# Kernel tuning notes

Hardware: AMD Instinct MI355X
Metric: run time of the kernel (lower is better)

The kernel has to match this reference:

```python
import jax, jax.numpy as jnp
import numpy as np

T, D, I, E, K = 2048, 768, 2048, 8, 2


def setup_inputs() -> dict:
    key = jax.random.key(0)
    ks = jax.random.split(key, 9)
    x = jax.random.normal(ks[0], (T, D), jnp.float32)
    router_weight = jax.random.normal(ks[1], (E, D), jnp.float32) * 0.02
    shared_w_gate = jax.random.normal(ks[2], (I, D), jnp.float32) * 0.02
    shared_w_up = jax.random.normal(ks[3], (I, D), jnp.float32) * 0.02
    shared_w_down = jax.random.normal(ks[4], (D, I), jnp.float32) * 0.02
    # ternary quantized expert weights in {-1, 0, 1}
    expert_q_gate = jax.random.randint(ks[5], (E, I, D), 0, 3, jnp.int32) - 1
    expert_q_up = jax.random.randint(ks[6], (E, I, D), 0, 3, jnp.int32) - 1
    expert_q_down = jax.random.randint(ks[7], (E, D, I), 0, 3, jnp.int32) - 1
    # per-expert, per-matrix dequant scales (gate, up, down)
    expert_scales = jax.random.uniform(ks[8], (E, 3), jnp.float32) * 0.05 + 0.01
    return {
        "x": x,
        "router_weight": router_weight,
        "shared_w_gate": shared_w_gate,
        "shared_w_up": shared_w_up,
        "shared_w_down": shared_w_down,
        "expert_q_gate": expert_q_gate,
        "expert_q_up": expert_q_up,
        "expert_q_down": expert_q_down,
        "expert_scales": expert_scales,
        "top_k": K,
    }


def _swiglu(x, wg, wu, wd):
    # down( silu(gate(x)) * up(x) )
    return (jax.nn.silu(x @ wg.T) * (x @ wu.T)) @ wd.T


def reference(x, router_weight, shared_w_gate, shared_w_up, shared_w_down,
              expert_q_gate, expert_q_up, expert_q_down, expert_scales, top_k):
    # --- router: softmax -> top-k -> renormalize ---
    probs = jax.nn.softmax(x @ router_weight.T, axis=-1)            # [T, E]
    vals, idx = jax.lax.top_k(probs, top_k)                          # [T, K]
    vals = vals / jnp.sum(vals, axis=-1, keepdims=True)
    n_experts = router_weight.shape[0]
    # combine weights as dense [T, E] gate (one-hot scatter of top-k probs)
    gate = jnp.sum(jax.nn.one_hot(idx, n_experts, dtype=x.dtype) * vals[..., None], axis=1)

    # --- dequantize paged ternary experts: w = ternary * scale ---
    wg = expert_q_gate.astype(x.dtype) * expert_scales[:, 0, None, None]  # [E, I, D]
    wu = expert_q_up.astype(x.dtype) * expert_scales[:, 1, None, None]    # [E, I, D]
    wd = expert_q_down.astype(x.dtype) * expert_scales[:, 2, None, None]  # [E, D, I]

    # --- expert SwiGLU, computed per expert and combined with the gate ---
    h = jax.nn.silu(jnp.einsum('td,eid->tei', x, wg)) * jnp.einsum('td,eid->tei', x, wu)
    expert_out = jnp.einsum('tei,edi->ted', h, wd)                   # [T, E, D]
    moe_out = jnp.einsum('te,ted->td', gate, expert_out)             # [T, D]

    # --- always-on shared expert ---
    shared_out = _swiglu(x, shared_w_gate, shared_w_up, shared_w_down)
    return shared_out + moe_out
```

## Files before the change

### kernel.cpp

```cpp
#include <hip/hip_runtime.h>
#include <hip/hip_bf16.h>

#define TDIM 2048
#define DDIM 768
#define IDIM 2048
#define NEXP 8

typedef __bf16 v8bf __attribute__((ext_vector_type(8)));
typedef float v4f __attribute__((ext_vector_type(4)));
typedef int   v4i __attribute__((ext_vector_type(4)));
typedef float v4ff __attribute__((ext_vector_type(4)));

#define MFMA_B16(A,B,C) __builtin_amdgcn_mfma_f32_16x16x32_bf16(A,B,C,0,0,0)

typedef __attribute__((address_space(1))) const unsigned int* gas_t;
typedef __attribute__((address_space(3))) unsigned int* las_t;

__device__ __forceinline__ void gload16(const void* g, void* l) {
  __builtin_amdgcn_global_load_lds((gas_t)g, (las_t)l, 16, 0, 0);
}

__global__ __launch_bounds__(256)
void pack_all_kernel(const int* __restrict__ qg, const int* __restrict__ qu,
                     const int* __restrict__ qd,
                     const float* __restrict__ sg, const float* __restrict__ su,
                     const float* __restrict__ sd, const float* __restrict__ x,
                     const float* __restrict__ rw,
                     __hip_bfloat16* __restrict__ wgT, __hip_bfloat16* __restrict__ wuT,
                     __hip_bfloat16* __restrict__ wdT, __hip_bfloat16* __restrict__ sgT,
                     __hip_bfloat16* __restrict__ suT, __hip_bfloat16* __restrict__ sdT,
                     __hip_bfloat16* __restrict__ xb,
                     int* __restrict__ cnt, int* __restrict__ lists, float* __restrict__ wt)
{
  const int b = blockIdx.x;
  const int tid = threadIdx.x;

  if (b < 512) {
    const int t = b * 4 + (tid >> 6);
    const int lane = tid & 63;
    const float* xp = x + (size_t)t * DDIM;
    float4 xv0 = *(const float4*)(xp + lane * 4);
    float4 xv1 = *(const float4*)(xp + 256 + lane * 4);
    float4 xv2 = *(const float4*)(xp + 512 + lane * 4);
    float logit[NEXP];
#pragma unroll
    for (int e = 0; e < NEXP; ++e) {
      const float* w = rw + (size_t)e * DDIM;
      float4 w0 = *(const float4*)(w + lane * 4);
      float4 w1 = *(const float4*)(w + 256 + lane * 4);
      float4 w2 = *(const float4*)(w + 512 + lane * 4);
      float p = xv0.x * w0.x + xv0.y * w0.y + xv0.z * w0.z + xv0.w * w0.w
              + xv1.x * w1.x + xv1.y * w1.y + xv1.z * w1.z + xv1.w * w1.w
              + xv2.x * w2.x + xv2.y * w2.y + xv2.z * w2.z + xv2.w * w2.w;
#pragma unroll
      for (int off = 32; off > 0; off >>= 1) p += __shfl_down(p, off, 64);
      logit[e] = p;
    }
    if (lane == 0) {
      float m = logit[0];
#pragma unroll
      for (int e = 1; e < NEXP; ++e) m = fmaxf(m, logit[e]);
      float pr[NEXP];
#pragma unroll
      for (int e = 0; e < NEXP; ++e) pr[e] = expf(logit[e] - m);
      int i0 = 0; float v0 = pr[0];
#pragma unroll
      for (int e = 1; e < NEXP; ++e) if (pr[e] > v0) { v0 = pr[e]; i0 = e; }
      int i1 = -1; float v1 = -1.f;
#pragma unroll
      for (int e = 0; e < NEXP; ++e) if (e != i0 && pr[e] > v1) { v1 = pr[e]; i1 = e; }
      float inv = 1.f / (v0 + v1);
      int p0 = atomicAdd(&cnt[i0], 1);
      lists[i0 * TDIM + p0] = t * 2;
      wt[t * 2] = v0 * inv;
      int p1 = atomicAdd(&cnt[i1], 1);
      lists[i1 * TDIM + p1] = t * 2 + 1;
      wt[t * 2 + 1] = v1 * inv;
    }
    return;
  }

  if (b < 1280) {
    const size_t i = (size_t)(b - 512) * 2048 + tid * 8;
    float4 a0 = *(const float4*)(x + i);
    float4 a1 = *(const float4*)(x + i + 4);
    v8bf v;
    v[0] = (__bf16)a0.x; v[1] = (__bf16)a0.y; v[2] = (__bf16)a0.z; v[3] = (__bf16)a0.w;
    v[4] = (__bf16)a1.x; v[5] = (__bf16)a1.y; v[6] = (__bf16)a1.z; v[7] = (__bf16)a1.w;
    *(v8bf*)(xb + i) = v;
    return;
  }

  const int wb = b - 1280;
  const void* src; __hip_bfloat16* dst; int NT, KT, isint, tile;
  if (wb < 1536)      { src = qg; dst = wgT; NT = 16; KT = 12; isint = 1; tile = wb; }
  else if (wb < 3072) { src = qu; dst = wuT; NT = 16; KT = 12; isint = 1; tile = wb - 1536; }
  else if (wb < 4608) { src = qd; dst = wdT; NT = 6;  KT = 32; isint = 1; tile = wb - 3072; }
  else if (wb < 4800) { src = sg; dst = sgT; NT = 16; KT = 12; isint = 0; tile = wb - 4608; }
  else if (wb < 4992) { src = su; dst = suT; NT = 16; KT = 12; isint = 0; tile = wb - 4800; }
  else                { src = sd; dst = sdT; NT = 6;  KT = 32; isint = 0; tile = wb - 4992; }
  const int kt = tile % KT;
  const int nt = (tile / KT) % NT;
  const int e  = tile / (KT * NT);
  const int Kk = KT * 64;

  const int row  = tid >> 1;
  const int half = tid & 1;
  const int xorm = (row & 7) << 4;
  const size_t srow = ((size_t)e * (NT * 128) + nt * 128 + row) * Kk + kt * 64;
  __hip_bfloat16* dptr = dst + (size_t)tile * 8192 + row * 64 + half * 32;

  if (isint) {
    const int* s = (const int*)src + srow;
    v4i r[8];
#pragma unroll
    for (int j = 0; j < 4; ++j) {
      const int k = ((half * 64 + j * 16) ^ xorm) >> 1;
      r[2 * j]     = __builtin_nontemporal_load((const v4i*)(s + k));
      r[2 * j + 1] = __builtin_nontemporal_load((const v4i*)(s + k) + 1);
    }
#pragma unroll
    for (int j = 0; j < 4; ++j) {
      v8bf v;
      v[0] = (__bf16)(float)r[2 * j][0];     v[1] = (__bf16)(float)r[2 * j][1];
      v[2] = (__bf16)(float)r[2 * j][2];     v[3] = (__bf16)(float)r[2 * j][3];
      v[4] = (__bf16)(float)r[2 * j + 1][0]; v[5] = (__bf16)(float)r[2 * j + 1][1];
      v[6] = (__bf16)(float)r[2 * j + 1][2]; v[7] = (__bf16)(float)r[2 * j + 1][3];
      *(v8bf*)(dptr + j * 8) = v;
    }
  } else {
    const float* s = (const float*)src + srow;
    v4ff r[8];
#pragma unroll
    for (int j = 0; j < 4; ++j) {
      const int k = ((half * 64 + j * 16) ^ xorm) >> 1;
      r[2 * j]     = *(const v4ff*)(s + k);
      r[2 * j + 1] = *((const v4ff*)(s + k) + 1);
    }
#pragma unroll
    for (int j = 0; j < 4; ++j) {
      v8bf v;
      v[0] = (__bf16)r[2 * j][0];     v[1] = (__bf16)r[2 * j][1];
      v[2] = (__bf16)r[2 * j][2];     v[3] = (__bf16)r[2 * j][3];
      v[4] = (__bf16)r[2 * j + 1][0]; v[5] = (__bf16)r[2 * j + 1][1];
      v[6] = (__bf16)r[2 * j + 1][2]; v[7] = (__bf16)r[2 * j + 1][3];
      *(v8bf*)(dptr + j * 8) = v;
    }
  }
}

__global__ __launch_bounds__(256, 3)
void gateup_kernel(const __hip_bfloat16* __restrict__ xb,
                   const __hip_bfloat16* __restrict__ wgT, const __hip_bfloat16* __restrict__ wuT,
                   const __hip_bfloat16* __restrict__ sgT, const __hip_bfloat16* __restrict__ suT,
                   const float* __restrict__ es,
                   const int* __restrict__ cnt, const int* __restrict__ lists,
                   __hip_bfloat16* __restrict__ he, __hip_bfloat16* __restrict__ hs)
{
  const int b = blockIdx.x;
  int tm, tn, count;
  const char *wg, *wu;
  const int* listE = nullptr;
  __hip_bfloat16* hout;
  float sg, su;
  if (b < 4096) {
    const int e = b >> 9; tm = (b >> 5) & 15; tn = b & 31;
    count = cnt[e];
    if (tm * 128 >= count) return;
    const size_t base = (size_t)(e * 16 + (tn >> 1)) * (12 * 16384) + (tn & 1) * 8192;
    wg = (const char*)wgT + base;
    wu = (const char*)wuT + base;
    listE = lists + e * TDIM;
    sg = es[e * 3 + 0]; su = es[e * 3 + 1];
    hout = he;
  } else {
    const int b2 = b - 4096; tm = b2 >> 5; tn = b2 & 31;
    count = TDIM;
    const size_t base = (size_t)(tn >> 1) * (12 * 16384) + (tn & 1) * 8192;
    wg = (const char*)sgT + base;
    wu = (const char*)suT + base;
    sg = 1.f; su = 1.f;
    hout = hs;
  }

  __shared__ __align__(16) char As[16384];
  __shared__ __align__(16) char Bg[8192];
  __shared__ __align__(16) char Bu[8192];

  const int tid = threadIdx.x;
  const int lane = tid & 63;
  const int wid = tid >> 6;
  const int wr = wid >> 1, wc = wid & 1;
  const int lr16 = lane & 15, hk = lane >> 4;

  const int cA = (((lane & 7) ^ (lane >> 3)) << 4);
  const char* aptr[4];
#pragma unroll
  for (int p = 0; p < 4; ++p) {
    const int row = p * 32 + wid * 8 + (lane >> 3);
    const int rg = tm * 128 + row;
    int tok;
    if (listE) { const int idx = rg < count ? rg : count - 1; tok = listE[idx] >> 1; }
    else tok = rg;
    aptr[p] = (const char*)xb + (size_t)tok * (DDIM * 2) + cA;
  }
  const char* bgp = wg + wid * 1024 + lane * 16;
  const char* bup = wu + wid * 1024 + lane * 16;
  char* ldsA  = As + wid * 1024;
  char* ldsBg = Bg + wid * 1024;
  char* ldsBu = Bu + wid * 1024;

  v4f ag[4][2] = {};
  v4f au[4][2] = {};

  for (int kt = 0; kt < 12; ++kt) {
#pragma unroll
    for (int p = 0; p < 4; ++p) gload16(aptr[p] + kt * 128, ldsA + p * 4096);
#pragma unroll
    for (int p = 0; p < 2; ++p) gload16(bgp + kt * 16384 + p * 4096, ldsBg + p * 4096);
#pragma unroll
    for (int p = 0; p < 2; ++p) gload16(bup + kt * 16384 + p * 4096, ldsBu + p * 4096);
    __syncthreads();
#pragma unroll
    for (int ks = 0; ks < 2; ++ks) {
      const int colb = ks * 64 + hk * 16;
      v8bf fa[4];
#pragma unroll
      for (int m = 0; m < 4; ++m) {
        const int r = wr * 64 + m * 16 + lr16;
        fa[m] = *(const v8bf*)(As + r * 128 + (colb ^ ((r & 7) << 4)));
      }
#pragma unroll
      for (int n = 0; n < 2; ++n) {
        const int r = wc * 32 + n * 16 + lr16;
        const int sb = r * 128 + (colb ^ ((r & 7) << 4));
        v8bf fg = *(const v8bf*)(Bg + sb);
        v8bf fu = *(const v8bf*)(Bu + sb);
#pragma unroll
        for (int m = 0; m < 4; ++m) {
          ag[m][n] = MFMA_B16(fa[m], fg, ag[m][n]);
          au[m][n] = MFMA_B16(fa[m], fu, au[m][n]);
        }
      }
    }
    __syncthreads();
  }

#pragma unroll
  for (int m = 0; m < 4; ++m) {
#pragma unroll
    for (int j = 0; j < 4; ++j) {
      const int rl = wr * 64 + m * 16 + hk * 4 + j;
      const int rg = tm * 128 + rl;
      if (rg >= count) continue;
      const size_t drow = listE ? (size_t)listE[rg] : (size_t)rg;
      __hip_bfloat16* dst = hout + drow * IDIM + tn * 64 + wc * 32 + lr16;
#pragma unroll
      for (int n = 0; n < 2; ++n) {
        const float g = ag[m][n][j] * sg;
        const float u = au[m][n][j] * su;
        const float h = g / (1.f + __expf(-g)) * u;
        dst[n * 16] = __float2bfloat16(h);
      }
    }
  }
}

__global__ __launch_bounds__(256, 4)
void down_kernel(const __hip_bfloat16* __restrict__ he, const __hip_bfloat16* __restrict__ hs,
                 const __hip_bfloat16* __restrict__ wdT, const __hip_bfloat16* __restrict__ sdT,
                 const float* __restrict__ es, const float* __restrict__ wt,
                 const int* __restrict__ cnt, const int* __restrict__ lists,
                 float* __restrict__ out)
{
  const int b = blockIdx.x;
  int tm, tn, count;
  const char* wd;
  const __hip_bfloat16* asrc;
  const int* listE = nullptr;
  float sd;
  if (b < 1536) {
    const int e = b / 192; const int r = b % 192; tm = r / 12; tn = r % 12;
    count = cnt[e];
    if (tm * 128 >= count) return;
    wd = (const char*)wdT + (size_t)(e * 6 + (tn >> 1)) * (32 * 16384) + (tn & 1) * 8192;
    listE = lists + e * TDIM;
    sd = es[e * 3 + 2];
    asrc = he;
  } else {
    const int r = b - 1536; tm = r / 12; tn = r % 12;
    count = TDIM;
    wd = (const char*)sdT + (size_t)(tn >> 1) * (32 * 16384) + (tn & 1) * 8192;
    sd = 1.f;
    asrc = hs;
  }

  __shared__ __align__(16) char As[16384];
  __shared__ __align__(16) char Bs[8192];

  const int tid = threadIdx.x;
  const int lane = tid & 63;
  const int wid = tid >> 6;
  const int wr = wid >> 1, wc = wid & 1;
  const int lr16 = lane & 15, hk = lane >> 4;

  const int cA = (((lane & 7) ^ (lane >> 3)) << 4);
  const char* aptr[4];
#pragma unroll
  for (int p = 0; p < 4; ++p) {
    const int row = p * 32 + wid * 8 + (lane >> 3);
    const int rg = tm * 128 + row;
    int srow;
    if (listE) { const int idx = rg < count ? rg : count - 1; srow = listE[idx]; }
    else srow = rg;
    aptr[p] = (const char*)asrc + (size_t)srow * (IDIM * 2) + cA;
  }
  const char* bp = wd + wid * 1024 + lane * 16;
  char* ldsA = As + wid * 1024;
  char* ldsB = Bs + wid * 1024;

  v4f acc[4][2] = {};

  for (int kt = 0; kt < 32; ++kt) {
#pragma unroll
    for (int p = 0; p < 4; ++p) gload16(aptr[p] + kt * 128, ldsA + p * 4096);
#pragma unroll
    for (int p = 0; p < 2; ++p) gload16(bp + kt * 16384 + p * 4096, ldsB + p * 4096);
    __syncthreads();
#pragma unroll
    for (int ks = 0; ks < 2; ++ks) {
      const int colb = ks * 64 + hk * 16;
      v8bf fa[4];
#pragma unroll
      for (int m = 0; m < 4; ++m) {
        const int r = wr * 64 + m * 16 + lr16;
        fa[m] = *(const v8bf*)(As + r * 128 + (colb ^ ((r & 7) << 4)));
      }
#pragma unroll
      for (int n = 0; n < 2; ++n) {
        const int r = wc * 32 + n * 16 + lr16;
        v8bf fb = *(const v8bf*)(Bs + r * 128 + (colb ^ ((r & 7) << 4)));
#pragma unroll
        for (int m = 0; m < 4; ++m) acc[m][n] = MFMA_B16(fa[m], fb, acc[m][n]);
      }
    }
    __syncthreads();
  }

#pragma unroll
  for (int m = 0; m < 4; ++m) {
#pragma unroll
    for (int j = 0; j < 4; ++j) {
      const int rl = wr * 64 + m * 16 + hk * 4 + j;
      const int rg = tm * 128 + rl;
      if (rg >= count) continue;
      int tok; float w;
      if (listE) { const int slot = listE[rg]; tok = slot >> 1; w = wt[slot] * sd; }
      else { tok = rg; w = 1.f; }
      float* dst = out + (size_t)tok * DDIM + tn * 64 + wc * 32 + lr16;
#pragma unroll
      for (int n = 0; n < 2; ++n) atomicAdd(dst + n * 16, acc[m][n][j] * w);
    }
  }
}

extern "C" void kernel_launch(void* const* d_in, const int* in_sizes, int n_in,
                              void* d_out, int out_size, void* d_ws, size_t ws_size,
                              hipStream_t stream)
{
  const float* x   = (const float*)d_in[0];
  const float* rw  = (const float*)d_in[1];
  const float* swg = (const float*)d_in[2];
  const float* swu = (const float*)d_in[3];
  const float* swd = (const float*)d_in[4];
  const int*   qg  = (const int*)d_in[5];
  const int*   qu  = (const int*)d_in[6];
  const int*   qd  = (const int*)d_in[7];
  const float* es  = (const float*)d_in[8];
  float* out = (float*)d_out;

  char* ws = (char*)d_ws;
  size_t off = 0;
  auto alloc = [&](size_t bytes) { void* p = ws + off; off = (off + bytes + 255) & ~(size_t)255; return p; };
  int*   cnt   = (int*)alloc(NEXP * 4);
  int*   lists = (int*)alloc((size_t)NEXP * TDIM * 4);
  float* wt    = (float*)alloc((size_t)2 * TDIM * 4);
  __hip_bfloat16* xb  = (__hip_bfloat16*)alloc((size_t)TDIM * DDIM * 2);
  __hip_bfloat16* wgT = (__hip_bfloat16*)alloc((size_t)NEXP * 16 * 12 * 8192 * 2);
  __hip_bfloat16* wuT = (__hip_bfloat16*)alloc((size_t)NEXP * 16 * 12 * 8192 * 2);
  __hip_bfloat16* wdT = (__hip_bfloat16*)alloc((size_t)NEXP * 6 * 32 * 8192 * 2);
  __hip_bfloat16* sgT = (__hip_bfloat16*)alloc((size_t)16 * 12 * 8192 * 2);
  __hip_bfloat16* suT = (__hip_bfloat16*)alloc((size_t)16 * 12 * 8192 * 2);
  __hip_bfloat16* sdT = (__hip_bfloat16*)alloc((size_t)6 * 32 * 8192 * 2);
  __hip_bfloat16* hs  = (__hip_bfloat16*)alloc((size_t)TDIM * IDIM * 2);
  __hip_bfloat16* he  = (__hip_bfloat16*)alloc((size_t)2 * TDIM * IDIM * 2);

  hipMemsetAsync(cnt, 0, NEXP * 4, stream);
  hipMemsetAsync(out, 0, (size_t)TDIM * DDIM * 4, stream);

  pack_all_kernel<<<512 + 768 + 5184, 256, 0, stream>>>(qg, qu, qd, swg, swu, swd, x, rw,
                                                        wgT, wuT, wdT, sgT, suT, sdT, xb,
                                                        cnt, lists, wt);

  gateup_kernel<<<4096 + 512, 256, 0, stream>>>(xb, wgT, wuT, sgT, suT, es, cnt, lists, he, hs);
  down_kernel<<<1536 + 192, 256, 0, stream>>>(he, hs, wdT, sdT, es, wt, cnt, lists, out);
}
```

Baseline: 428.6 us.

## Interleave gate/up weights into one packed B tile and widen down GEMM tiles

The pack kernel now writes gate and up rows interleaved in 16-row groups into a single packed buffer, so the gate/up GEMM loads one 128-wide B tile and pairs adjacent accumulators for SiLU*up. The down GEMM switches from 128x64 to 128x128 tiles, halving block count and the number of times each A tile is reloaded. Expert and shared activations are merged into one h buffer, and the down-proj scale is folded into the routing weight. Each thread now holds 16 accumulators in both GEMMs, which raises register pressure and, with 3 blocks per CU, may cut occupancy for the down kernel.

```diff
diff --git a/kernel.cpp b/kernel.cpp
--- a/kernel.cpp
+++ b/kernel.cpp
@@ -25,10 +25,9 @@
                      const int* __restrict__ qd,
                      const float* __restrict__ sg, const float* __restrict__ su,
                      const float* __restrict__ sd, const float* __restrict__ x,
-                     const float* __restrict__ rw,
-                     __hip_bfloat16* __restrict__ wgT, __hip_bfloat16* __restrict__ wuT,
-                     __hip_bfloat16* __restrict__ wdT, __hip_bfloat16* __restrict__ sgT,
-                     __hip_bfloat16* __restrict__ suT, __hip_bfloat16* __restrict__ sdT,
+                     const float* __restrict__ rw, const float* __restrict__ es,
+                     __hip_bfloat16* __restrict__ wguT, __hip_bfloat16* __restrict__ sguT,
+                     __hip_bfloat16* __restrict__ wdT,  __hip_bfloat16* __restrict__ sdT,
                      __hip_bfloat16* __restrict__ xb,
                      int* __restrict__ cnt, int* __restrict__ lists, float* __restrict__ wt)
 {
@@ -72,10 +71,10 @@
       float inv = 1.f / (v0 + v1);
       int p0 = atomicAdd(&cnt[i0], 1);
       lists[i0 * TDIM + p0] = t * 2;
-      wt[t * 2] = v0 * inv;
+      wt[t * 2] = v0 * inv * es[i0 * 3 + 2];
       int p1 = atomicAdd(&cnt[i1], 1);
       lists[i1 * TDIM + p1] = t * 2 + 1;
-      wt[t * 2 + 1] = v1 * inv;
+      wt[t * 2 + 1] = v1 * inv * es[i1 * 3 + 2];
     }
     return;
   }
@@ -92,100 +91,108 @@
   }
 
   const int wb = b - 1280;
-  const void* src; __hip_bfloat16* dst; int NT, KT, isint, tile;
-  if (wb < 1536)      { src = qg; dst = wgT; NT = 16; KT = 12; isint = 1; tile = wb; }
-  else if (wb < 3072) { src = qu; dst = wuT; NT = 16; KT = 12; isint = 1; tile = wb - 1536; }
-  else if (wb < 4608) { src = qd; dst = wdT; NT = 6;  KT = 32; isint = 1; tile = wb - 3072; }
-  else if (wb < 4800) { src = sg; dst = sgT; NT = 16; KT = 12; isint = 0; tile = wb - 4608; }
-  else if (wb < 4992) { src = su; dst = suT; NT = 16; KT = 12; isint = 0; tile = wb - 4800; }
-  else                { src = sd; dst = sdT; NT = 6;  KT = 32; isint = 0; tile = wb - 4992; }
-  const int kt = tile % KT;
-  const int nt = (tile / KT) % NT;
-  const int e  = tile / (KT * NT);
-  const int Kk = KT * 64;
-
-  const int row  = tid >> 1;
-  const int half = tid & 1;
-  const int xorm = (row & 7) << 4;
-  const size_t srow = ((size_t)e * (NT * 128) + nt * 128 + row) * Kk + kt * 64;
-  __hip_bfloat16* dptr = dst + (size_t)tile * 8192 + row * 64 + half * 32;
+  const char *sA, *sB;
+  __hip_bfloat16* dst;
+  int tnt, kt, isint, paired;
+  size_t K;
+  if (wb < 3072) {
+    const int e = wb / 384, rem = wb % 384; tnt = rem / 12; kt = rem % 12;
+    sA = (const char*)(qg + (size_t)e * IDIM * DDIM);
+    sB = (const char*)(qu + (size_t)e * IDIM * DDIM);
+    dst = wguT + (size_t)wb * 8192; isint = 1; paired = 1; K = DDIM;
+  } else if (wb < 3456) {
+    const int tg = wb - 3072; tnt = tg / 12; kt = tg % 12;
+    sA = (const char*)sg; sB = (const char*)su;
+    dst = sguT + (size_t)tg * 8192; isint = 0; paired = 1; K = DDIM;
+  } else if (wb < 4992) {
+    const int tg = wb - 3456; const int e = tg / 192, rem = tg % 192; tnt = rem / 32; kt = rem % 32;
+    sA = (const char*)(qd + (size_t)e * DDIM * IDIM); sB = sA;
+    dst = wdT + (size_t)tg * 8192; isint = 1; paired = 0; K = IDIM;
+  } else {
+    const int tg = wb - 4992; tnt = tg / 32; kt = tg % 32;
+    sA = (const char*)sd; sB = sA;
+    dst = sdT + (size_t)tg * 8192; isint = 0; paired = 0; K = IDIM;
+  }
+
+  const char* sp[4];
+  int qidx[4];
+#pragma unroll
+  for (int p = 0; p < 4; ++p) {
+    const int q = p * 256 + tid;
+    const int row = q >> 3;
+    const int cb = ((q & 7) * 16) ^ ((row & 7) << 4);
+    const int rg = tnt * 128 + row;
+    int srcrow, which;
+    if (paired) { which = (rg >> 4) & 1; srcrow = (rg >> 5) * 16 + (rg & 15); }
+    else        { which = 0; srcrow = rg; }
+    const char* base = which ? sB : sA;
+    sp[p] = base + ((size_t)srcrow * K + kt * 64 + (cb >> 1)) * 4;
+    qidx[p] = q;
+  }
 
   if (isint) {
-    const int* s = (const int*)src + srow;
     v4i r[8];
 #pragma unroll
-    for (int j = 0; j < 4; ++j) {
-      const int k = ((half * 64 + j * 16) ^ xorm) >> 1;
-      r[2 * j]     = __builtin_nontemporal_load((const v4i*)(s + k));
-      r[2 * j + 1] = __builtin_nontemporal_load((const v4i*)(s + k) + 1);
-    }
-#pragma unroll
-    for (int j = 0; j < 4; ++j) {
+    for (int p = 0; p < 4; ++p) {
+      r[2 * p]     = *(const v4i*)sp[p];
+      r[2 * p + 1] = *((const v4i*)sp[p] + 1);
+    }
+#pragma unroll
+    for (int p = 0; p < 4; ++p) {
       v8bf v;
-      v[0] = (__bf16)(float)r[2 * j][0];     v[1] = (__bf16)(float)r[2 * j][1];
-      v[2] = (__bf16)(float)r[2 * j][2];     v[3] = (__bf16)(float)r[2 * j][3];
-      v[4] = (__bf16)(float)r[2 * j + 1][0]; v[5] = (__bf16)(float)r[2 * j + 1][1];
-      v[6] = (__bf16)(float)r[2 * j + 1][2]; v[7] = (__bf16)(float)r[2 * j + 1][3];
-      *(v8bf*)(dptr + j * 8) = v;
+      v[0] = (__bf16)(float)r[2 * p][0];     v[1] = (__bf16)(float)r[2 * p][1];
+      v[2] = (__bf16)(float)r[2 * p][2];     v[3] = (__bf16)(float)r[2 * p][3];
+      v[4] = (__bf16)(float)r[2 * p + 1][0]; v[5] = (__bf16)(float)r[2 * p + 1][1];
+      v[6] = (__bf16)(float)r[2 * p + 1][2]; v[7] = (__bf16)(float)r[2 * p + 1][3];
+      *(v8bf*)(dst + (size_t)qidx[p] * 8) = v;
     }
   } else {
-    const float* s = (const float*)src + srow;
     v4ff r[8];
 #pragma unroll
-    for (int j = 0; j < 4; ++j) {
-      const int k = ((half * 64 + j * 16) ^ xorm) >> 1;
-      r[2 * j]     = *(const v4ff*)(s + k);
-      r[2 * j + 1] = *((const v4ff*)(s + k) + 1);
-    }
-#pragma unroll
-    for (int j = 0; j < 4; ++j) {
+    for (int p = 0; p < 4; ++p) {
+      r[2 * p]     = *(const v4ff*)sp[p];
+      r[2 * p + 1] = *((const v4ff*)sp[p] + 1);
+    }
+#pragma unroll
+    for (int p = 0; p < 4; ++p) {
       v8bf v;
-      v[0] = (__bf16)r[2 * j][0];     v[1] = (__bf16)r[2 * j][1];
-      v[2] = (__bf16)r[2 * j][2];     v[3] = (__bf16)r[2 * j][3];
-      v[4] = (__bf16)r[2 * j + 1][0]; v[5] = (__bf16)r[2 * j + 1][1];
-      v[6] = (__bf16)r[2 * j + 1][2]; v[7] = (__bf16)r[2 * j + 1][3];
-      *(v8bf*)(dptr + j * 8) = v;
+      v[0] = (__bf16)r[2 * p][0];     v[1] = (__bf16)r[2 * p][1];
+      v[2] = (__bf16)r[2 * p][2];     v[3] = (__bf16)r[2 * p][3];
+      v[4] = (__bf16)r[2 * p + 1][0]; v[5] = (__bf16)r[2 * p + 1][1];
+      v[6] = (__bf16)r[2 * p + 1][2]; v[7] = (__bf16)r[2 * p + 1][3];
+      *(v8bf*)(dst + (size_t)qidx[p] * 8) = v;
     }
   }
 }
 
 __global__ __launch_bounds__(256, 3)
-void gateup_kernel(const __hip_bfloat16* __restrict__ xb,
-                   const __hip_bfloat16* __restrict__ wgT, const __hip_bfloat16* __restrict__ wuT,
-                   const __hip_bfloat16* __restrict__ sgT, const __hip_bfloat16* __restrict__ suT,
-                   const float* __restrict__ es,
-                   const int* __restrict__ cnt, const int* __restrict__ lists,
-                   __hip_bfloat16* __restrict__ he, __hip_bfloat16* __restrict__ hs)
+void gu_gemm_kernel(const __hip_bfloat16* __restrict__ xb,
+                    const __hip_bfloat16* __restrict__ wguT, const __hip_bfloat16* __restrict__ sguT,
+                    const float* __restrict__ es,
+                    const int* __restrict__ cnt, const int* __restrict__ lists,
+                    __hip_bfloat16* __restrict__ h)
 {
   const int b = blockIdx.x;
   int tm, tn, count;
-  const char *wg, *wu;
+  const char* bbase;
   const int* listE = nullptr;
-  __hip_bfloat16* hout;
-  float sg, su;
+  float sgc, suc;
   if (b < 4096) {
     const int e = b >> 9; tm = (b >> 5) & 15; tn = b & 31;
     count = cnt[e];
     if (tm * 128 >= count) return;
-    const size_t base = (size_t)(e * 16 + (tn >> 1)) * (12 * 16384) + (tn & 1) * 8192;
-    wg = (const char*)wgT + base;
-    wu = (const char*)wuT + base;
+    bbase = (const char*)wguT + (size_t)(e * 32 + tn) * (12 * 16384);
     listE = lists + e * TDIM;
-    sg = es[e * 3 + 0]; su = es[e * 3 + 1];
-    hout = he;
+    sgc = es[e * 3 + 0]; suc = es[e * 3 + 1];
   } else {
     const int b2 = b - 4096; tm = b2 >> 5; tn = b2 & 31;
     count = TDIM;
-    const size_t base = (size_t)(tn >> 1) * (12 * 16384) + (tn & 1) * 8192;
-    wg = (const char*)sgT + base;
-    wu = (const char*)suT + base;
-    sg = 1.f; su = 1.f;
-    hout = hs;
+    bbase = (const char*)sguT + (size_t)tn * (12 * 16384);
+    sgc = 1.f; suc = 1.f;
   }
 
   __shared__ __align__(16) char As[16384];
-  __shared__ __align__(16) char Bg[8192];
-  __shared__ __align__(16) char Bu[8192];
+  __shared__ __align__(16) char Bs[16384];
 
   const int tid = threadIdx.x;
   const int lane = tid & 63;
@@ -204,44 +211,34 @@
     else tok = rg;
     aptr[p] = (const char*)xb + (size_t)tok * (DDIM * 2) + cA;
   }
-  const char* bgp = wg + wid * 1024 + lane * 16;
-  const char* bup = wu + wid * 1024 + lane * 16;
-  char* ldsA  = As + wid * 1024;
-  char* ldsBg = Bg + wid * 1024;
-  char* ldsBu = Bu + wid * 1024;
-
-  v4f ag[4][2] = {};
-  v4f au[4][2] = {};
+  const char* bp = bbase + wid * 1024 + lane * 16;
+
+  v4f acc[4][4] = {};
 
   for (int kt = 0; kt < 12; ++kt) {
 #pragma unroll
-    for (int p = 0; p < 4; ++p) gload16(aptr[p] + kt * 128, ldsA + p * 4096);
-#pragma unroll
-    for (int p = 0; p < 2; ++p) gload16(bgp + kt * 16384 + p * 4096, ldsBg + p * 4096);
-#pragma unroll
-    for (int p = 0; p < 2; ++p) gload16(bup + kt * 16384 + p * 4096, ldsBu + p * 4096);
+    for (int p = 0; p < 4; ++p) gload16(aptr[p] + kt * 128, As + wid * 1024 + p * 4096);
+#pragma unroll
+    for (int p = 0; p < 4; ++p) gload16(bp + kt * 16384 + p * 4096, Bs + wid * 1024 + p * 4096);
     __syncthreads();
 #pragma unroll
     for (int ks = 0; ks < 2; ++ks) {
       const int colb = ks * 64 + hk * 16;
-      v8bf fa[4];
+      v8bf fa[4], fb[4];
 #pragma unroll
       for (int m = 0; m < 4; ++m) {
         const int r = wr * 64 + m * 16 + lr16;
         fa[m] = *(const v8bf*)(As + r * 128 + (colb ^ ((r & 7) << 4)));
       }
 #pragma unroll
-      for (int n = 0; n < 2; ++n) {
-        const int r = wc * 32 + n * 16 + lr16;
-        const int sb = r * 128 + (colb ^ ((r & 7) << 4));
-        v8bf fg = *(const v8bf*)(Bg + sb);
-        v8bf fu = *(const v8bf*)(Bu + sb);
-#pragma unroll
-        for (int m = 0; m < 4; ++m) {
-          ag[m][n] = MFMA_B16(fa[m], fg, ag[m][n]);
-          au[m][n] = MFMA_B16(fa[m], fu, au[m][n]);
-        }
-      }
+      for (int n = 0; n < 4; ++n) {
+        const int r = wc * 64 + n * 16 + lr16;
+        fb[n] = *(const v8bf*)(Bs + r * 128 + (colb ^ ((r & 7) << 4)));
+      }
+#pragma unroll
+      for (int n = 0; n < 4; ++n)
+#pragma unroll
+        for (int m = 0; m < 4; ++m) acc[m][n] = MFMA_B16(fa[m], fb[n], acc[m][n]);
     }
     __syncthreads();
   }
@@ -253,50 +250,43 @@
       const int rl = wr * 64 + m * 16 + hk * 4 + j;
       const int rg = tm * 128 + rl;
       if (rg >= count) continue;
-      const size_t drow = listE ? (size_t)listE[rg] : (size_t)rg;
-      __hip_bfloat16* dst = hout + drow * IDIM + tn * 64 + wc * 32 + lr16;
-#pragma unroll
-      for (int n = 0; n < 2; ++n) {
-        const float g = ag[m][n][j] * sg;
-        const float u = au[m][n][j] * su;
-        const float h = g / (1.f + __expf(-g)) * u;
-        dst[n * 16] = __float2bfloat16(h);
-      }
-    }
-  }
-}
-
-__global__ __launch_bounds__(256, 4)
-void down_kernel(const __hip_bfloat16* __restrict__ he, const __hip_bfloat16* __restrict__ hs,
+      const size_t drow = listE ? (size_t)listE[rg] : (size_t)(4096 + rg);
+      __hip_bfloat16* dh = h + drow * IDIM + (tn * 4 + wc * 2) * 16 + lr16;
+#pragma unroll
+      for (int p = 0; p < 2; ++p) {
+        const float g = acc[m][2 * p][j] * sgc;
+        const float u = acc[m][2 * p + 1][j] * suc;
+        dh[p * 16] = __float2bfloat16(g / (1.f + __expf(-g)) * u);
+      }
+    }
+  }
+}
+
+__global__ __launch_bounds__(256, 3)
+void down_kernel(const __hip_bfloat16* __restrict__ h,
                  const __hip_bfloat16* __restrict__ wdT, const __hip_bfloat16* __restrict__ sdT,
-                 const float* __restrict__ es, const float* __restrict__ wt,
+                 const float* __restrict__ wt,
                  const int* __restrict__ cnt, const int* __restrict__ lists,
                  float* __restrict__ out)
 {
   const int b = blockIdx.x;
   int tm, tn, count;
-  const char* wd;
-  const __hip_bfloat16* asrc;
+  const char* bbase;
   const int* listE = nullptr;
-  float sd;
-  if (b < 1536) {
-    const int e = b / 192; const int r = b % 192; tm = r / 12; tn = r % 12;
+  if (b < 768) {
+    const int e = b / 96; const int r = b % 96; tm = r / 6; tn = r % 6;
     count = cnt[e];
     if (tm * 128 >= count) return;
-    wd = (const char*)wdT + (size_t)(e * 6 + (tn >> 1)) * (32 * 16384) + (tn & 1) * 8192;
+    bbase = (const char*)wdT + (size_t)(e * 6 + tn) * (32 * 16384);
     listE = lists + e * TDIM;
-    sd = es[e * 3 + 2];
-    asrc = he;
   } else {
-    const int r = b - 1536; tm = r / 12; tn = r % 12;
+    const int r = b - 768; tm = r / 6; tn = r % 6;
     count = TDIM;
-    wd = (const char*)sdT + (size_t)(tn >> 1) * (32 * 16384) + (tn & 1) * 8192;
-    sd = 1.f;
-    asrc = hs;
+    bbase = (const char*)sdT + (size_t)tn * (32 * 16384);
   }
 
   __shared__ __align__(16) char As[16384];
-  __shared__ __align__(16) char Bs[8192];
+  __shared__ __align__(16) char Bs[16384];
 
   const int tid = threadIdx.x;
   const int lane = tid & 63;
@@ -312,37 +302,37 @@
     const int rg = tm * 128 + row;
     int srow;
     if (listE) { const int idx = rg < count ? rg : count - 1; srow = listE[idx]; }
-    else srow = rg;
-    aptr[p] = (const char*)asrc + (size_t)srow * (IDIM * 2) + cA;
-  }
-  const char* bp = wd + wid * 1024 + lane * 16;
-  char* ldsA = As + wid * 1024;
-  char* ldsB = Bs + wid * 1024;
-
-  v4f acc[4][2] = {};
+    else srow = 4096 + rg;
+    aptr[p] = (const char*)h + (size_t)srow * (IDIM * 2) + cA;
+  }
+  const char* bp = bbase + wid * 1024 + lane * 16;
+
+  v4f acc[4][4] = {};
 
   for (int kt = 0; kt < 32; ++kt) {
 #pragma unroll
-    for (int p = 0; p < 4; ++p) gload16(aptr[p] + kt * 128, ldsA + p * 4096);
-#pragma unroll
-    for (int p = 0; p < 2; ++p) gload16(bp + kt * 16384 + p * 4096, ldsB + p * 4096);
+    for (int p = 0; p < 4; ++p) gload16(aptr[p] + kt * 128, As + wid * 1024 + p * 4096);
+#pragma unroll
+    for (int p = 0; p < 4; ++p) gload16(bp + kt * 16384 + p * 4096, Bs + wid * 1024 + p * 4096);
     __syncthreads();
 #pragma unroll
     for (int ks = 0; ks < 2; ++ks) {
       const int colb = ks * 64 + hk * 16;
-      v8bf fa[4];
+      v8bf fa[4], fb[4];
 #pragma unroll
       for (int m = 0; m < 4; ++m) {
         const int r = wr * 64 + m * 16 + lr16;
         fa[m] = *(const v8bf*)(As + r * 128 + (colb ^ ((r & 7) << 4)));
       }
 #pragma unroll
-      for (int n = 0; n < 2; ++n) {
-        const int r = wc * 32 + n * 16 + lr16;
-        v8bf fb = *(const v8bf*)(Bs + r * 128 + (colb ^ ((r & 7) << 4)));
-#pragma unroll
-        for (int m = 0; m < 4; ++m) acc[m][n] = MFMA_B16(fa[m], fb, acc[m][n]);
-      }
+      for (int n = 0; n < 4; ++n) {
+        const int r = wc * 64 + n * 16 + lr16;
+        fb[n] = *(const v8bf*)(Bs + r * 128 + (colb ^ ((r & 7) << 4)));
+      }
+#pragma unroll
+      for (int n = 0; n < 4; ++n)
+#pragma unroll
+        for (int m = 0; m < 4; ++m) acc[m][n] = MFMA_B16(fa[m], fb[n], acc[m][n]);
     }
     __syncthreads();
   }
@@ -355,11 +345,11 @@
       const int rg = tm * 128 + rl;
       if (rg >= count) continue;
       int tok; float w;
-      if (listE) { const int slot = listE[rg]; tok = slot >> 1; w = wt[slot] * sd; }
+      if (listE) { const int slot = listE[rg]; tok = slot >> 1; w = wt[slot]; }
       else { tok = rg; w = 1.f; }
-      float* dst = out + (size_t)tok * DDIM + tn * 64 + wc * 32 + lr16;
-#pragma unroll
-      for (int n = 0; n < 2; ++n) atomicAdd(dst + n * 16, acc[m][n][j] * w);
+      float* dst = out + (size_t)tok * DDIM + tn * 128 + wc * 64 + lr16;
+#pragma unroll
+      for (int n = 0; n < 4; ++n) atomicAdd(dst + n * 16, acc[m][n][j] * w);
     }
   }
 }
@@ -385,23 +375,18 @@
   int*   cnt   = (int*)alloc(NEXP * 4);
   int*   lists = (int*)alloc((size_t)NEXP * TDIM * 4);
   float* wt    = (float*)alloc((size_t)2 * TDIM * 4);
-  __hip_bfloat16* xb  = (__hip_bfloat16*)alloc((size_t)TDIM * DDIM * 2);
-  __hip_bfloat16* wgT = (__hip_bfloat16*)alloc((size_t)NEXP * 16 * 12 * 8192 * 2);
-  __hip_bfloat16* wuT = (__hip_bfloat16*)alloc((size_t)NEXP * 16 * 12 * 8192 * 2);
-  __hip_bfloat16* wdT = (__hip_bfloat16*)alloc((size_t)NEXP * 6 * 32 * 8192 * 2);
-  __hip_bfloat16* sgT = (__hip_bfloat16*)alloc((size_t)16 * 12 * 8192 * 2);
-  __hip_bfloat16* suT = (__hip_bfloat16*)alloc((size_t)16 * 12 * 8192 * 2);
-  __hip_bfloat16* sdT = (__hip_bfloat16*)alloc((size_t)6 * 32 * 8192 * 2);
-  __hip_bfloat16* hs  = (__hip_bfloat16*)alloc((size_t)TDIM * IDIM * 2);
-  __hip_bfloat16* he  = (__hip_bfloat16*)alloc((size_t)2 * TDIM * IDIM * 2);
+  __hip_bfloat16* xb   = (__hip_bfloat16*)alloc((size_t)TDIM * DDIM * 2);
+  __hip_bfloat16* wguT = (__hip_bfloat16*)alloc((size_t)NEXP * 32 * 12 * 8192 * 2);
+  __hip_bfloat16* sguT = (__hip_bfloat16*)alloc((size_t)32 * 12 * 8192 * 2);
+  __hip_bfloat16* wdT  = (__hip_bfloat16*)alloc((size_t)NEXP * 6 * 32 * 8192 * 2);
+  __hip_bfloat16* sdT  = (__hip_bfloat16*)alloc((size_t)6 * 32 * 8192 * 2);
+  __hip_bfloat16* h    = (__hip_bfloat16*)alloc((size_t)(4096 + TDIM) * IDIM * 2);
 
   hipMemsetAsync(cnt, 0, NEXP * 4, stream);
   hipMemsetAsync(out, 0, (size_t)TDIM * DDIM * 4, stream);
 
-  pack_all_kernel<<<512 + 768 + 5184, 256, 0, stream>>>(qg, qu, qd, swg, swu, swd, x, rw,
-                                                        wgT, wuT, wdT, sgT, suT, sdT, xb,
-                                                        cnt, lists, wt);
-
-  gateup_kernel<<<4096 + 512, 256, 0, stream>>>(xb, wgT, wuT, sgT, suT, es, cnt, lists, he, hs);
-  down_kernel<<<1536 + 192, 256, 0, stream>>>(he, hs, wdT, sdT, es, wt, cnt, lists, out);
-}
+  pack_all_kernel<<<6464, 256, 0, stream>>>(qg, qu, qd, swg, swu, swd, x, rw, es,
+                                            wguT, sguT, wdT, sdT, xb, cnt, lists, wt);
+  gu_gemm_kernel<<<4096 + 512, 256, 0, stream>>>(xb, wguT, sguT, es, cnt, lists, h);
+  down_kernel<<<768 + 96, 256, 0, stream>>>(h, wdT, sdT, wt, cnt, lists, out);
+}
```

Measured after the change: 347.6 us. 1.23x faster.
